# Optimization experiments

Hardware: AMD Instinct MI355X
Metric: run time of the kernel (lower is better)

## Reference

```python
import jax, jax.numpy as jnp
import numpy as np

B, C, N, M, H, L = 2, 128, 6000, 1500, 4, 3
DH = C // H


def conv1(x, W, b):
    # 1x1 Conv1d == per-position matmul: x [B,Cin,N], W [Cout,Cin], b [Cout]
    return jnp.einsum('oc,bcn->bon', W, x) + b[None, :, None]


def setup_inputs():
    key = jax.random.key(0)
    ks = jax.random.split(key, 16)
    w = lambda k, shape, fan: (jax.random.normal(k, shape, jnp.float32) / np.sqrt(fan)).astype(jnp.float32)
    inp = {
        'xs': jax.random.normal(ks[0], (B, 1, N, 4), jnp.float32),
        'd': jax.random.normal(ks[1], (B, C, N), jnp.float32),
        'feat_piece': jax.random.normal(ks[2], (B, C, M), jnp.float32),
        'logits_in': jax.random.normal(ks[3], (B, N), jnp.float32),
        'Wq': w(ks[4], (L, C, C), C), 'bq': jnp.zeros((L, C), jnp.float32),
        'Wk': w(ks[5], (L, C, C), C), 'bk': jnp.zeros((L, C), jnp.float32),
        'Wv': w(ks[6], (L, C, C), C), 'bv': jnp.zeros((L, C), jnp.float32),
        'Wm': w(ks[7], (L, C, C), C), 'bm': jnp.zeros((L, C), jnp.float32),
        'Wc1': w(ks[8], (L, 2 * C, 2 * C), 2 * C), 'bc1': jnp.zeros((L, 2 * C), jnp.float32),
        'bns': jnp.ones((L, 2 * C), jnp.float32), 'bnsh': jnp.zeros((L, 2 * C), jnp.float32),
        'Wc2': w(ks[9], (L, C, 2 * C), 2 * C), 'bc2': jnp.zeros((L, C), jnp.float32),
        'iW1': w(ks[10], (64, C), C), 'ib1': jnp.zeros((64,), jnp.float32),
        'ibn1s': jnp.ones((64,), jnp.float32), 'ibn1sh': jnp.zeros((64,), jnp.float32),
        'iW2': w(ks[11], (16, 64), 64), 'ib2': jnp.zeros((16,), jnp.float32),
        'ibn2s': jnp.ones((16,), jnp.float32), 'ibn2sh': jnp.zeros((16,), jnp.float32),
        'iW3': w(ks[12], (4, 16), 16), 'ib3': jnp.zeros((4,), jnp.float32),
        'ibn3s': jnp.ones((4,), jnp.float32), 'ibn3sh': jnp.zeros((4,), jnp.float32),
        'iW4': w(ks[13], (1, 4), 4), 'ib4': jnp.zeros((1,), jnp.float32),
    }
    return inp


def _forward(xs, d, feat_piece, logits_in, Wq, bq, Wk, bk, Wv, bv, Wm, bm, Wc1, bc1, bns, bnsh, Wc2, bc2,
             iW1, ib1, ibn1s, ibn1sh, iW2, ib2, ibn2s, ibn2sh, iW3, ib3, ibn3s, ibn3sh, iW4, ib4):
    d_old = d
    # kv_mask = (relu(tanh(logits)) > 0) == (logits > 0)
    mask = logits_in > 0.0

    def attention(x1, x2, kv_mask, i):
        bsz = x1.shape[0]
        q = conv1(x1, Wq[i], bq[i]).reshape(bsz, H, DH, -1)  # [B,H,Dh,Nq]
        k = conv1(x2, Wk[i], bk[i]).reshape(bsz, H, DH, -1)  # [B,H,Dh,Nk]
        v = conv1(x2, Wv[i], bv[i]).reshape(bsz, H, DH, -1)
        QK = jnp.einsum('bhdn,bhdm->bhnm', q, k)
        if kv_mask is not None:
            # masked_fill BEFORE the sqrt(head_dim) scaling, as in the original
            QK = jnp.where(kv_mask[:, None, None, :], QK, jnp.float32(-1e6))
        score = jax.nn.softmax(QK / jnp.float32(np.sqrt(DH)), axis=-1)
        add = jnp.einsum('bhnm,bhdm->bhdn', score, v).reshape(bsz, C, -1)
        add = conv1(add, Wm[i], bm[i])
        h = conv1(jnp.concatenate([x1, add], axis=1), Wc1[i], bc1[i])
        # BatchNorm1d (eval) folded into per-channel scale/shift, then ReLU
        h = jax.nn.relu(h * bns[i][None, :, None] + bnsh[i][None, :, None])
        return x1 + conv1(h, Wc2[i], bc2[i])

    feat = attention(feat_piece, d, mask, 0)   # 'cluster':   feat_piece <- d (masked kv)
    feat = attention(feat, feat, None, 1)      # 'context':   self-attention
    d = attention(d, feat, None, 2)            # 'decluster': d <- feat_piece

    def inst_norm(x, eps=1e-3):
        mu = jnp.mean(x, axis=-1, keepdims=True)
        var = jnp.var(x, axis=-1, keepdims=True)  # biased, matches InstanceNorm1d
        return (x - mu) / jnp.sqrt(var + eps)

    def block(x, W, b, s, sh):
        x = inst_norm(conv1(x, W, b))
        return jax.nn.relu(x * s[None, :, None] + sh[None, :, None])

    x = d - d_old
    x = block(x, iW1, ib1, ibn1s, ibn1sh)
    x = block(x, iW2, ib2, ibn2s, ibn2sh)
    x = block(x, iW3, ib3, ibn3s, ibn3sh)
    logits = conv1(x, iW4, ib4)[:, 0, :]  # squeeze channel dim -> [B,N]
    return d, logits  # e_hat is None (loss=False path)


def reference(xs, d, feat_piece, logits_in, Wq, bq, Wk, bk, Wv, bv, Wm, bm, Wc1, bc1, bns, bnsh, Wc2, bc2,
              iW1, ib1, ibn1s, ibn1sh, iW2, ib2, ibn2s, ibn2sh, iW3, ib3, ibn3s, ibn3sh, iW4, ib4):
    return _forward(xs, d, feat_piece, logits_in, Wq, bq, Wk, bk, Wv, bv, Wm, bm, Wc1, bc1, bns, bnsh, Wc2, bc2,
                    iW1, ib1, ibn1s, ibn1sh, iW2, ib2, ibn2s, ibn2sh, iW3, ib3, ibn3s, ibn3sh, iW4, ib4)
```

## Files before the change

kernel.cpp:

```cpp
#include <hip/hip_runtime.h>
#include <math.h>

#define B_  2
#define C_  128
#define N_  6000
#define M_  1500
#define H_  4
#define DH_ 32

typedef __attribute__((ext_vector_type(8))) short bf16x8;
typedef __attribute__((ext_vector_type(4))) float f32x4;
typedef unsigned short u16;

static __device__ __forceinline__ u16 f2bf(float x) {
    unsigned u = __float_as_uint(x);
    return (u16)((u + 0x7fffu + ((u >> 16) & 1u)) >> 16);
}
#define MFMA(a,b,c) __builtin_amdgcn_mfma_f32_16x16x32_bf16((a),(b),(c),0,0,0)
#define INVS2 (0.17677669529663687f * 1.4426950408889634f)

__global__ __launch_bounds__(256) void prep_kernel(
    const float* __restrict__ Wq, const float* __restrict__ Wk, const float* __restrict__ Wv,
    const float* __restrict__ Wm, const float* __restrict__ Wc1, const float* __restrict__ Wc2,
    const float* __restrict__ iW1,
    u16* __restrict__ wq, u16* __restrict__ wk, u16* __restrict__ wv, u16* __restrict__ wm,
    u16* __restrict__ wc1, u16* __restrict__ wc2, u16* __restrict__ w1,
    float* __restrict__ zstats)
{
    long i = (long)blockIdx.x * 256 + threadIdx.x;
    if (i < 512)    zstats[i] = 0.f;
    if (i < 49152)  { wq[i] = f2bf(Wq[i]); wk[i] = f2bf(Wk[i]);
                      wv[i] = f2bf(Wv[i]); wm[i] = f2bf(Wm[i]); }
    if (i < 196608) wc1[i] = f2bf(Wc1[i]);
    if (i < 98304)  wc2[i] = f2bf(Wc2[i]);
    if (i < 8192)   w1[i]  = f2bf(iW1[i]);
}

__global__ __launch_bounds__(256) void qkv_kernel(
    const float* __restrict__ x1, const float* __restrict__ x2, int Pq, int Pk, int Pkpad,
    const u16* __restrict__ wq, const u16* __restrict__ wk, const u16* __restrict__ wv,
    const float* __restrict__ bq, const float* __restrict__ bk, const float* __restrict__ bv,
    u16* __restrict__ Q16, u16* __restrict__ K16, u16* __restrict__ V16)
{
    __shared__ u16 Xt[64][40];
    const int tid = threadIdx.x;
    const int wid = tid >> 6, lane = tid & 63;
    const int l15 = lane & 15, quad = lane >> 4;
    const int job = blockIdx.y >> 1, ot = blockIdx.y & 1;
    const int b = blockIdx.z;
    const int p0 = blockIdx.x * 64;
    const float* X; const u16* W; const float* bias; u16* Y; int P;
    if (job == 0)      { X = x1; W = wq; bias = bq; Y = Q16; P = Pq; }
    else if (job == 1) { X = x2; W = wk; bias = bk; Y = K16; P = Pk; }
    else               { X = x2; W = wv; bias = bv; Y = V16; P = Pk; }
    if (p0 >= P) return;
    const long xoff = (long)b * C_ * P;
    const int sp = tid & 63, cg = tid >> 6;
    f32x4 acc[4] = {};

    for (int k0 = 0; k0 < 128; k0 += 32) {
        bf16x8 st;
        {
            const int pp = (p0 + sp < P) ? p0 + sp : P - 1;
            #pragma unroll
            for (int j = 0; j < 8; ++j)
                st[j] = (short)f2bf(X[xoff + (long)(k0 + cg * 8 + j) * P + pp]);
        }
        __syncthreads();
        *(bf16x8*)&Xt[sp][cg * 8] = st;
        __syncthreads();
        const bf16x8 af = *(const bf16x8*)(W + (long)(ot * 64 + wid * 16 + l15) * 128 + k0 + quad * 8);
        #pragma unroll
        for (int pg = 0; pg < 4; ++pg) {
            const bf16x8 bfr = *(const bf16x8*)&Xt[pg * 16 + l15][quad * 8];
            acc[pg] = MFMA(af, bfr, acc[pg]);
        }
    }
    #pragma unroll
    for (int pg = 0; pg < 4; ++pg)
        #pragma unroll
        for (int r = 0; r < 4; ++r) {
            const int o = ot * 64 + wid * 16 + quad * 4 + r;
            const int p = p0 + pg * 16 + l15;
            if (p < P) {
                const u16 v = f2bf(acc[pg][r] + bias[o]);
                if (job <= 1)
                    Y[((long)(b * 4 + (o >> 5)) * P + p) * 32 + (o & 31)] = v;
                else
                    Y[(long)(b * 128 + o) * Pkpad + p] = v;
            }
        }
}

__global__ __launch_bounds__(256) void attn_partial(
    const u16* __restrict__ Q16, const u16* __restrict__ K16, const u16* __restrict__ V16,
    const float* __restrict__ lgin,
    float* __restrict__ pl, float* __restrict__ pacc,
    int Nq, int Nk, int Nkpad, int KS, int chunkLen)
{
    __shared__ u16 Ps[4][32][72];
    const int tid  = threadIdx.x;
    const int wave = tid >> 6, lane = tid & 63;
    const int l15  = lane & 15, quad = lane >> 4;
    const int bid  = blockIdx.x;
    const int bh   = bid & 7, rest = bid >> 3;
    const int split = rest % KS, qblk = rest / KS;
    const int b = bh >> 2;
    const int q0w = qblk * 128 + wave * 32;

    const u16* Qb = Q16 + (long)bh * Nq * 32;
    const u16* Kb = K16 + (long)bh * Nk * 32;
    const u16* Vb = V16 + (long)(bh * 32) * Nkpad;

    const int qq0 = min(q0w + l15, Nq - 1);
    const int qq1 = min(q0w + 16 + l15, Nq - 1);
    const bf16x8 qa0 = *(const bf16x8*)(Qb + (long)qq0 * 32 + quad * 8);
    const bf16x8 qa1 = *(const bf16x8*)(Qb + (long)qq1 * 32 + quad * 8);

    float lp0 = 0.f, lp1 = 0.f;
    f32x4 o00 = {0.f,0.f,0.f,0.f}, o01 = {0.f,0.f,0.f,0.f};
    f32x4 o10 = {0.f,0.f,0.f,0.f}, o11 = {0.f,0.f,0.f,0.f};

    const int kbeg = split * chunkLen;
    const int kend = min(Nk, kbeg + chunkLen);
    const f32x4 z4 = {0.f,0.f,0.f,0.f};

    for (int m0 = kbeg; m0 < kend; m0 += 64) {
        f32x4 sa0[4], sa1[4];
        #pragma unroll
        for (int kg = 0; kg < 4; ++kg) {
            const int krow = min(m0 + kg * 16 + l15, Nk - 1);
            const bf16x8 ka = *(const bf16x8*)(Kb + (long)krow * 32 + quad * 8);
            sa0[kg] = MFMA(ka, qa0, z4);
            sa1[kg] = MFMA(ka, qa1, z4);
        }

        const int kedge = kend - m0;
        #pragma unroll
        for (int kg = 0; kg < 4; ++kg) {
            float4 mv = {1.f, 1.f, 1.f, 1.f};
            if (lgin)
                mv = *(const float4*)&lgin[(long)b * Nk + min(m0 + kg * 16 + quad * 4, Nk - 4)];
            const float* mr = (const float*)&mv;
            unsigned lo0, hi0, lo1, hi1;
            float p0[4], p1[4];
            #pragma unroll
            for (int r = 0; r < 4; ++r) {
                const bool good = (kg * 16 + quad * 4 + r < kedge) && (mr[r] > 0.f);
                p0[r] = good ? exp2f(sa0[kg][r] * INVS2) : 0.f;
                p1[r] = good ? exp2f(sa1[kg][r] * INVS2) : 0.f;
            }
            lp0 += (p0[0] + p0[1]) + (p0[2] + p0[3]);
            lp1 += (p1[0] + p1[1]) + (p1[2] + p1[3]);
            lo0 = (unsigned)f2bf(p0[0]) | ((unsigned)f2bf(p0[1]) << 16);
            hi0 = (unsigned)f2bf(p0[2]) | ((unsigned)f2bf(p0[3]) << 16);
            lo1 = (unsigned)f2bf(p1[0]) | ((unsigned)f2bf(p1[1]) << 16);
            hi1 = (unsigned)f2bf(p1[2]) | ((unsigned)f2bf(p1[3]) << 16);
            *(uint2*)&Ps[wave][l15][kg * 16 + quad * 4]      = make_uint2(lo0, hi0);
            *(uint2*)&Ps[wave][16 + l15][kg * 16 + quad * 4] = make_uint2(lo1, hi1);
        }

        const bf16x8 pa0lo = *(const bf16x8*)&Ps[wave][l15][quad * 8];
        const bf16x8 pa0hi = *(const bf16x8*)&Ps[wave][l15][32 + quad * 8];
        const bf16x8 pa1lo = *(const bf16x8*)&Ps[wave][16 + l15][quad * 8];
        const bf16x8 pa1hi = *(const bf16x8*)&Ps[wave][16 + l15][32 + quad * 8];
        #pragma unroll
        for (int dg = 0; dg < 2; ++dg) {
            const u16* vrow = Vb + (long)(dg * 16 + l15) * Nkpad + m0;
            const bf16x8 vblo = *(const bf16x8*)(vrow + quad * 8);
            const bf16x8 vbhi = *(const bf16x8*)(vrow + 32 + quad * 8);
            if (dg == 0) {
                o00 = MFMA(pa0lo, vblo, o00); o00 = MFMA(pa0hi, vbhi, o00);
                o10 = MFMA(pa1lo, vblo, o10); o10 = MFMA(pa1hi, vbhi, o10);
            } else {
                o01 = MFMA(pa0lo, vblo, o01); o01 = MFMA(pa0hi, vbhi, o01);
                o11 = MFMA(pa1lo, vblo, o11); o11 = MFMA(pa1hi, vbhi, o11);
            }
        }
    }

    lp0 += __shfl_xor(lp0, 16); lp0 += __shfl_xor(lp0, 32);
    lp1 += __shfl_xor(lp1, 16); lp1 += __shfl_xor(lp1, 32);

    const long base = (long)bh * KS + split;
    if (quad == 0) {
        const int qa = q0w + l15, qbq = q0w + 16 + l15;
        if (qa  < Nq) pl[base * Nq + qa]  = lp0;
        if (qbq < Nq) pl[base * Nq + qbq] = lp1;
    }
    #pragma unroll
    for (int r = 0; r < 4; ++r) {
        const int qa = q0w + quad * 4 + r;
        const int qbq = q0w + 16 + quad * 4 + r;
        if (qa < Nq) {
            float* dst = &pacc[((long)base * Nq + qa) * 32];
            dst[l15] = o00[r]; dst[16 + l15] = o01[r];
        }
        if (qbq < Nq) {
            float* dst = &pacc[((long)base * Nq + qbq) * 32];
            dst[l15] = o10[r]; dst[16 + l15] = o11[r];
        }
    }
}

__global__ __launch_bounds__(256) void epi_kernel(
    const float* __restrict__ pl, const float* __restrict__ pacc, int KS,
    const float* __restrict__ x1,
    const u16* __restrict__ Wm, const float* __restrict__ bm,
    const u16* __restrict__ Wc1, const float* __restrict__ bc1,
    const float* __restrict__ bns, const float* __restrict__ bnsh,
    const u16* __restrict__ Wc2, const float* __restrict__ bc2,
    float* __restrict__ outF, float* __restrict__ outR, int Nq)
{
    __shared__ u16 Xa[32][136];
    __shared__ u16 Xc[32][264];
    __shared__ u16 Xh[32][264];
    const int tid = threadIdx.x;
    const int wid = tid >> 6, lane = tid & 63;
    const int l15 = lane & 15, quad = lane >> 4;
    const int b = blockIdx.y;
    const int p0 = blockIdx.x * 32;

    {
        const int pos = tid & 31, sub = tid >> 5;
        const int pp = (p0 + pos < Nq) ? p0 + pos : Nq - 1;
        const int h = sub >> 1, d0 = (sub & 1) * 16;
        const int bh = b * 4 + h;
        float lg = 0.f, acc[16];
        #pragma unroll
        for (int i = 0; i < 16; ++i) acc[i] = 0.f;
        for (int s = 0; s < KS; ++s) {
            const long base = (long)bh * KS + s;
            lg += pl[base * Nq + pp];
            const float* src = &pacc[(base * Nq + pp) * 32 + d0];
            #pragma unroll
            for (int i = 0; i < 4; ++i) {
                const float4 v = *(const float4*)&src[i * 4];
                acc[i*4+0] += v.x; acc[i*4+1] += v.y; acc[i*4+2] += v.z; acc[i*4+3] += v.w;
            }
        }
        const float inv = 1.f / lg;
        bf16x8 v0, v1;
        #pragma unroll
        for (int i = 0; i < 8; ++i) { v0[i] = (short)f2bf(acc[i] * inv); v1[i] = (short)f2bf(acc[8 + i] * inv); }
        const int c0 = h * 32 + (sub & 1) * 16;
        *(bf16x8*)&Xa[pos][c0] = v0;
        *(bf16x8*)&Xa[pos][c0 + 8] = v1;
        bf16x8 y0, y1;
        #pragma unroll
        for (int j = 0; j < 8; ++j) {
            y0[j] = (short)f2bf(x1[((long)b * 128 + sub * 16 + j) * Nq + pp]);
            y1[j] = (short)f2bf(x1[((long)b * 128 + sub * 16 + 8 + j) * Nq + pp]);
        }
        *(bf16x8*)&Xc[pos][sub * 16] = y0;
        *(bf16x8*)&Xc[pos][sub * 16 + 8] = y1;
    }
    __syncthreads();

    {
        f32x4 am[2][2] = {};
        for (int k0 = 0; k0 < 128; k0 += 32) {
            #pragma unroll
            for (int og = 0; og < 2; ++og) {
                const bf16x8 af = *(const bf16x8*)(Wm + (long)(wid * 32 + og * 16 + l15) * 128 + k0 + quad * 8);
                #pragma unroll
                for (int pg = 0; pg < 2; ++pg) {
                    const bf16x8 bfr = *(const bf16x8*)&Xa[pg * 16 + l15][k0 + quad * 8];
                    am[og][pg] = MFMA(af, bfr, am[og][pg]);
                }
            }
        }
        #pragma unroll
        for (int og = 0; og < 2; ++og)
            #pragma unroll
            for (int pg = 0; pg < 2; ++pg)
                #pragma unroll
                for (int r = 0; r < 4; ++r) {
                    const int o = wid * 32 + og * 16 + quad * 4 + r;
                    Xc[pg * 16 + l15][128 + o] = f2bf(am[og][pg][r] + bm[o]);
                }
    }
    __syncthreads();

    {
        f32x4 a1[4][2] = {};
        for (int k0 = 0; k0 < 256; k0 += 32) {
            #pragma unroll
            for (int og = 0; og < 4; ++og) {
                const bf16x8 af = *(const bf16x8*)(Wc1 + (long)(wid * 64 + og * 16 + l15) * 256 + k0 + quad * 8);
                #pragma unroll
                for (int pg = 0; pg < 2; ++pg) {
                    const bf16x8 bfr = *(const bf16x8*)&Xc[pg * 16 + l15][k0 + quad * 8];
                    a1[og][pg] = MFMA(af, bfr, a1[og][pg]);
                }
            }
        }
        #pragma unroll
        for (int og = 0; og < 4; ++og)
            #pragma unroll
            for (int pg = 0; pg < 2; ++pg)
                #pragma unroll
                for (int r = 0; r < 4; ++r) {
                    const int o = wid * 64 + og * 16 + quad * 4 + r;
                    const float hv = fmaxf((a1[og][pg][r] + bc1[o]) * bns[o] + bnsh[o], 0.f);
                    Xh[pg * 16 + l15][o] = f2bf(hv);
                }
    }
    __syncthreads();

    {
        f32x4 a2[2][2] = {};
        for (int k0 = 0; k0 < 256; k0 += 32) {
            #pragma unroll
            for (int og = 0; og < 2; ++og) {
                const bf16x8 af = *(const bf16x8*)(Wc2 + (long)(wid * 32 + og * 16 + l15) * 256 + k0 + quad * 8);
                #pragma unroll
                for (int pg = 0; pg < 2; ++pg) {
                    const bf16x8 bfr = *(const bf16x8*)&Xh[pg * 16 + l15][k0 + quad * 8];
                    a2[og][pg] = MFMA(af, bfr, a2[og][pg]);
                }
            }
        }
        #pragma unroll
        for (int og = 0; og < 2; ++og)
            #pragma unroll
            for (int pg = 0; pg < 2; ++pg)
                #pragma unroll
                for (int r = 0; r < 4; ++r) {
                    const int o = wid * 32 + og * 16 + quad * 4 + r;
                    const int p = p0 + pg * 16 + l15;
                    if (p < Nq) {
                        const long idx = ((long)b * 128 + o) * Nq + p;
                        const float v = a2[og][pg][r] + bc2[o];
                        outF[idx] = v + x1[idx];
                        if (outR) outR[idx] = v;
                    }
                }
    }
}

__global__ __launch_bounds__(256) void tail1_kernel(
    const float* __restrict__ X, const u16* __restrict__ W, const float* __restrict__ bias,
    float* __restrict__ Y, float* __restrict__ ps, float* __restrict__ pq, int P)
{
    __shared__ u16 Xt[64][40];
    const int tid = threadIdx.x;
    const int wid = tid >> 6, lane = tid & 63;
    const int l15 = lane & 15, quad = lane >> 4;
    const int b = blockIdx.y;
    const int p0 = blockIdx.x * 64;
    const int sp = tid & 63, cg = tid >> 6;
    f32x4 acc[4] = {};
    for (int k0 = 0; k0 < 128; k0 += 32) {
        bf16x8 st;
        {
            const int pp = (p0 + sp < P) ? p0 + sp : P - 1;
            #pragma unroll
            for (int j = 0; j < 8; ++j)
                st[j] = (short)f2bf(X[((long)b * 128 + k0 + cg * 8 + j) * P + pp]);
        }
        __syncthreads();
        *(bf16x8*)&Xt[sp][cg * 8] = st;
        __syncthreads();
        const bf16x8 af = *(const bf16x8*)(W + (long)(wid * 16 + l15) * 128 + k0 + quad * 8);
        #pragma unroll
        for (int pg = 0; pg < 4; ++pg) {
            const bf16x8 bfr = *(const bf16x8*)&Xt[pg * 16 + l15][quad * 8];
            acc[pg] = MFMA(af, bfr, acc[pg]);
        }
    }
    float sums[4] = {}, sq[4] = {};
    #pragma unroll
    for (int pg = 0; pg < 4; ++pg)
        #pragma unroll
        for (int r = 0; r < 4; ++r) {
            const int o = wid * 16 + quad * 4 + r;
            const int p = p0 + pg * 16 + l15;
            if (p < P) {
                const float v = acc[pg][r] + bias[o];
                Y[((long)b * 64 + o) * P + p] = v;
                sums[r] += v; sq[r] += v * v;
            }
        }
    #pragma unroll
    for (int mk = 1; mk < 16; mk <<= 1)
        #pragma unroll
        for (int r = 0; r < 4; ++r) { sums[r] += __shfl_xor(sums[r], mk); sq[r] += __shfl_xor(sq[r], mk); }
    if (l15 == 0)
        #pragma unroll
        for (int r = 0; r < 4; ++r) {
            const int o = wid * 16 + quad * 4 + r;
            atomicAdd(&ps[b * 64 + o], sums[r]);
            atomicAdd(&pq[b * 64 + o], sq[r]);
        }
}

template<int CI, int CO>
__global__ __launch_bounds__(256) void tail_mid(
    const float* __restrict__ xraw, const float* __restrict__ ps, const float* __restrict__ pq,
    const float* __restrict__ sc, const float* __restrict__ sh,
    const float* __restrict__ W, const float* __restrict__ bias,
    float* __restrict__ ps2, float* __restrict__ pq2, float* __restrict__ yraw, int P)
{
    __shared__ float k1s[CI], k2s[CI], Wl[CO * CI];
    const int tid = threadIdx.x;
    const int b = blockIdx.y;
    for (int i = tid; i < CO * CI; i += 256) Wl[i] = W[i];
    if (tid < CI) {
        const float S = ps[b * CI + tid], Q2 = pq[b * CI + tid];
        const float mu = S / P;
        const float var = Q2 / P - mu * mu;
        const float rs = rsqrtf(var + 1e-3f);
        k1s[tid] = rs * sc[tid];
        k2s[tid] = sh[tid] - mu * rs * sc[tid];
    }
    __syncthreads();
    const int p = blockIdx.x * 256 + tid;
    const bool valid = p < P;
    const int pp = valid ? p : P - 1;
    float acc[CO];
    #pragma unroll
    for (int o = 0; o < CO; ++o) acc[o] = bias[o];
    for (int c = 0; c < CI; ++c) {
        const float xn = fmaxf(xraw[((long)b * CI + c) * P + pp] * k1s[c] + k2s[c], 0.f);
        #pragma unroll
        for (int o = 0; o < CO; ++o) acc[o] += Wl[o * CI + c] * xn;
    }
    float sums[CO], sq[CO];
    #pragma unroll
    for (int o = 0; o < CO; ++o) {
        const float v = acc[o];
        if (valid) yraw[((long)b * CO + o) * P + p] = v;
        sums[o] = valid ? v : 0.f;
        sq[o] = valid ? v * v : 0.f;
    }
    #pragma unroll
    for (int mk = 1; mk < 64; mk <<= 1)
        #pragma unroll
        for (int o = 0; o < CO; ++o) { sums[o] += __shfl_xor(sums[o], mk); sq[o] += __shfl_xor(sq[o], mk); }
    if ((tid & 63) == 0)
        #pragma unroll
        for (int o = 0; o < CO; ++o) {
            atomicAdd(&ps2[b * CO + o], sums[o]);
            atomicAdd(&pq2[b * CO + o], sq[o]);
        }
}

__global__ __launch_bounds__(256) void tail4_kernel(
    const float* __restrict__ xraw, const float* __restrict__ ps, const float* __restrict__ pq,
    const float* __restrict__ sc, const float* __restrict__ sh,
    const float* __restrict__ W4, const float* __restrict__ b4,
    float* __restrict__ out, int P)
{
    const int tid = threadIdx.x;
    const int b = blockIdx.y;
    const int p = blockIdx.x * 256 + tid;
    if (p >= P) return;
    float acc = b4[0];
    #pragma unroll
    for (int c = 0; c < 4; ++c) {
        const float S = ps[b * 4 + c], Q2 = pq[b * 4 + c];
        const float mu = S / P;
        const float var = Q2 / P - mu * mu;
        const float rs = rsqrtf(var + 1e-3f);
        const float k1 = rs * sc[c], k2 = sh[c] - mu * rs * sc[c];
        const float xn = fmaxf(xraw[((long)b * 4 + c) * P + p] * k1 + k2, 0.f);
        acc += W4[c] * xn;
    }
    out[(long)b * P + p] = acc;
}

extern "C" void kernel_launch(void* const* d_in, const int* in_sizes, int n_in,
                              void* d_out, int out_size, void* d_ws, size_t ws_size,
                              hipStream_t stream)
{
    const float* dX   = (const float*)d_in[1];
    const float* fpX  = (const float*)d_in[2];
    const float* lgin = (const float*)d_in[3];
    const float* Wq = (const float*)d_in[4];  const float* bq = (const float*)d_in[5];
    const float* Wk = (const float*)d_in[6];  const float* bk = (const float*)d_in[7];
    const float* Wv = (const float*)d_in[8];  const float* bv = (const float*)d_in[9];
    const float* Wm = (const float*)d_in[10]; const float* bm = (const float*)d_in[11];
    const float* Wc1= (const float*)d_in[12]; const float* bc1= (const float*)d_in[13];
    const float* bns= (const float*)d_in[14]; const float* bnsh=(const float*)d_in[15];
    const float* Wc2= (const float*)d_in[16]; const float* bc2= (const float*)d_in[17];
    const float* iW1= (const float*)d_in[18]; const float* ib1= (const float*)d_in[19];
    const float* s1 = (const float*)d_in[20]; const float* h1 = (const float*)d_in[21];
    const float* iW2= (const float*)d_in[22]; const float* ib2= (const float*)d_in[23];
    const float* s2 = (const float*)d_in[24]; const float* h2 = (const float*)d_in[25];
    const float* iW3= (const float*)d_in[26]; const float* ib3= (const float*)d_in[27];
    const float* s3 = (const float*)d_in[28]; const float* h3 = (const float*)d_in[29];
    const float* iW4= (const float*)d_in[30]; const float* ib4= (const float*)d_in[31];

    float* out_d      = (float*)d_out;
    float* out_logits = out_d + (long)B_ * C_ * N_;

    float* f = (float*)d_ws;
    long off = 0;
    auto alloc = [&](long n) { float* p = f + off; off += n; return p; };
    float* featA = alloc(384000);
    float* featB = alloc(384000);
    float* q16f  = alloc(800000);
    float* k16f  = alloc(800000);
    float* v16f  = alloc(800000);
    float* xb    = alloc(1536000);
    float* x1raw = alloc(768000);
    float* x2raw = alloc(192000);
    float* x3raw = alloc(48000);
    float* plb   = alloc(100000);
    float* pacc  = alloc(3200000);
    float* zst   = alloc(512);
    float* wreg  = alloc(250000);
    (void)ws_size; (void)in_sizes; (void)n_in; (void)out_size;

    float* ps1 = zst;        float* pq1 = zst + 128;
    float* ps2 = zst + 256;  float* pq2 = zst + 288;
    float* ps3 = zst + 320;  float* pq3 = zst + 328;

    u16* wq_h  = (u16*)wreg;
    u16* wk_h  = wq_h + 49152;
    u16* wv_h  = wk_h + 49152;
    u16* wm_h  = wv_h + 49152;
    u16* wc1_h = wm_h + 49152;
    u16* wc2_h = wc1_h + 196608;
    u16* w1_h  = wc2_h + 98304;

    u16* Q16 = (u16*)q16f;
    u16* K16 = (u16*)k16f;
    u16* V16 = (u16*)v16f;

    prep_kernel<<<dim3(768), 256, 0, stream>>>(Wq, Wk, Wv, Wm, Wc1, Wc2, iW1,
                                               wq_h, wk_h, wv_h, wm_h, wc1_h, wc2_h, w1_h, zst);

    auto layer = [&](const float* x1, const float* x2, int Nq, int Nk,
                     const float* maskl, int li, int KS, int chunkLen,
                     float* outF, float* outR) {
        const int Nkpad = ((Nk + 63) & ~63) + 64;
        qkv_kernel<<<dim3((max(Nq, Nk) + 63) / 64, 6, B_), 256, 0, stream>>>(
            x1, x2, Nq, Nk, Nkpad,
            wq_h + (long)li * 16384, wk_h + (long)li * 16384, wv_h + (long)li * 16384,
            bq + li * 128, bk + li * 128, bv + li * 128, Q16, K16, V16);
        const int qblocks = (Nq + 127) / 128;
        attn_partial<<<dim3(qblocks * KS * 8), 256, 0, stream>>>(
            Q16, K16, V16, maskl, plb, pacc, Nq, Nk, Nkpad, KS, chunkLen);
        epi_kernel<<<dim3((Nq + 31) / 32, B_), 256, 0, stream>>>(
            plb, pacc, KS, x1,
            wm_h + (long)li * 16384, bm + li * 128,
            wc1_h + (long)li * 65536, bc1 + li * 256, bns + li * 256, bnsh + li * 256,
            wc2_h + (long)li * 32768, bc2 + li * 128,
            outF, outR, Nq);
    };

    layer(fpX,   dX,    M_, N_, lgin,    0, 8, 768, featA, nullptr);
    layer(featA, featA, M_, M_, nullptr, 1, 8, 192, featB, nullptr);
    layer(dX,    featB, N_, M_, nullptr, 2, 2, 768, out_d, xb);

    tail1_kernel<<<dim3((N_ + 63) / 64, B_), 256, 0, stream>>>(xb, w1_h, ib1, x1raw, ps1, pq1, N_);
    tail_mid<64, 16><<<dim3((N_ + 255) / 256, B_), 256, 0, stream>>>(
        x1raw, ps1, pq1, s1, h1, iW2, ib2, ps2, pq2, x2raw, N_);
    tail_mid<16, 4><<<dim3((N_ + 255) / 256, B_), 256, 0, stream>>>(
        x2raw, ps2, pq2, s2, h2, iW3, ib3, ps3, pq3, x3raw, N_);
    tail4_kernel<<<dim3((N_ + 255) / 256, B_), 256, 0, stream>>>(
        x3raw, ps3, pq3, s3, h3, iW4, ib4, out_logits, N_);
}
```

Baseline: 397.8 us.

## Pad K/V to chunk multiple, fold softmax scale into Q, row sums via MFMA

The QKV projection now pre-scales Q by the softmax/log2 factor and writes K and V zero-padded to KS*chunkLen. V gets an extra block of rows with a ones row appended. The attention kernel drops the per-element bounds clamps and scale multiply, uses a template to skip the mask path when unmasked, and truncates P to bf16 instead of rounding it. Row sums are computed with extra MFMAs against a ones fragment instead of VALU adds and shuffles, with padded keys subtracted as npad (exp(0)=1). This trades more memory traffic, extra MFMAs and a slight precision change for less VALU work in the inner loop.

```diff
diff --git a/kernel.cpp b/kernel.cpp
--- a/kernel.cpp
+++ b/kernel.cpp
@@ -49,54 +49,71 @@
     const int job = blockIdx.y >> 1, ot = blockIdx.y & 1;
     const int b = blockIdx.z;
     const int p0 = blockIdx.x * 64;
-    const float* X; const u16* W; const float* bias; u16* Y; int P;
-    if (job == 0)      { X = x1; W = wq; bias = bq; Y = Q16; P = Pq; }
-    else if (job == 1) { X = x2; W = wk; bias = bk; Y = K16; P = Pk; }
-    else               { X = x2; W = wv; bias = bv; Y = V16; P = Pk; }
-    if (p0 >= P) return;
-    const long xoff = (long)b * C_ * P;
-    const int sp = tid & 63, cg = tid >> 6;
-    f32x4 acc[4] = {};
-
-    for (int k0 = 0; k0 < 128; k0 += 32) {
-        bf16x8 st;
-        {
-            const int pp = (p0 + sp < P) ? p0 + sp : P - 1;
-            #pragma unroll
-            for (int j = 0; j < 8; ++j)
-                st[j] = (short)f2bf(X[xoff + (long)(k0 + cg * 8 + j) * P + pp]);
-        }
-        __syncthreads();
-        *(bf16x8*)&Xt[sp][cg * 8] = st;
-        __syncthreads();
-        const bf16x8 af = *(const bf16x8*)(W + (long)(ot * 64 + wid * 16 + l15) * 128 + k0 + quad * 8);
-        #pragma unroll
-        for (int pg = 0; pg < 4; ++pg) {
-            const bf16x8 bfr = *(const bf16x8*)&Xt[pg * 16 + l15][quad * 8];
-            acc[pg] = MFMA(af, bfr, acc[pg]);
-        }
-    }
-    #pragma unroll
-    for (int pg = 0; pg < 4; ++pg)
-        #pragma unroll
-        for (int r = 0; r < 4; ++r) {
-            const int o = ot * 64 + wid * 16 + quad * 4 + r;
-            const int p = p0 + pg * 16 + l15;
-            if (p < P) {
-                const u16 v = f2bf(acc[pg][r] + bias[o]);
-                if (job <= 1)
-                    Y[((long)(b * 4 + (o >> 5)) * P + p) * 32 + (o & 31)] = v;
-                else
-                    Y[(long)(b * 128 + o) * Pkpad + p] = v;
-            }
-        }
-}
-
+    const float* X; const u16* W; const float* bias; int P;
+    if (job == 0)      { X = x1; W = wq; bias = bq; P = Pq; }
+    else if (job == 1) { X = x2; W = wk; bias = bk; P = Pk; }
+    else               { X = x2; W = wv; bias = bv; P = Pk; }
+    const int Plim = (job == 0) ? Pq : Pkpad;
+    if (p0 < Plim) {
+        const long xoff = (long)b * C_ * P;
+        const int sp = tid & 63, cg = tid >> 6;
+        f32x4 acc[4] = {};
+        if (p0 < P) {
+            for (int k0 = 0; k0 < 128; k0 += 32) {
+                bf16x8 st;
+                const int pp = (p0 + sp < P) ? p0 + sp : P - 1;
+                #pragma unroll
+                for (int j = 0; j < 8; ++j)
+                    st[j] = (short)f2bf(X[xoff + (long)(k0 + cg * 8 + j) * P + pp]);
+                __syncthreads();
+                *(bf16x8*)&Xt[sp][cg * 8] = st;
+                __syncthreads();
+                const bf16x8 af = *(const bf16x8*)(W + (long)(ot * 64 + wid * 16 + l15) * 128 + k0 + quad * 8);
+                #pragma unroll
+                for (int pg = 0; pg < 4; ++pg) {
+                    const bf16x8 bfr = *(const bf16x8*)&Xt[pg * 16 + l15][quad * 8];
+                    acc[pg] = MFMA(af, bfr, acc[pg]);
+                }
+            }
+        }
+        #pragma unroll
+        for (int pg = 0; pg < 4; ++pg)
+            #pragma unroll
+            for (int r = 0; r < 4; ++r) {
+                const int o = ot * 64 + wid * 16 + quad * 4 + r;
+                const int p = p0 + pg * 16 + l15;
+                if (p >= Plim) continue;
+                if (job == 0) {
+                    if (p < Pq)
+                        Q16[((long)(b * 4 + (o >> 5)) * Pq + p) * 32 + (o & 31)] =
+                            f2bf((acc[pg][r] + bias[o]) * INVS2);
+                } else {
+                    const u16 v = (p < P) ? f2bf(acc[pg][r] + bias[o]) : (u16)0;
+                    if (job == 1)
+                        K16[((long)(b * 4 + (o >> 5)) * Pkpad + p) * 32 + (o & 31)] = v;
+                    else
+                        V16[((long)(b * 4 + (o >> 5)) * 48 + (o & 31)) * Pkpad + p] = v;
+                }
+            }
+        if (job == 2) {
+            for (int e = tid; e < 2048; e += 256) {
+                const int which = e >> 10;
+                const int row = 32 + ((e >> 6) & 15);
+                const int col = p0 + (e & 63);
+                if (col < Pkpad)
+                    V16[((long)(b * 4 + ot * 2 + which) * 48 + row) * Pkpad + col] =
+                        (row == 32) ? (u16)0x3F80 : (u16)0;
+            }
+        }
+    }
+}
+
+template<bool MASKED>
 __global__ __launch_bounds__(256) void attn_partial(
     const u16* __restrict__ Q16, const u16* __restrict__ K16, const u16* __restrict__ V16,
     const float* __restrict__ lgin,
     float* __restrict__ pl, float* __restrict__ pacc,
-    int Nq, int Nk, int Nkpad, int KS, int chunkLen)
+    int Nq, int Nk, int Nkpad, int KS, int chunkLen, int npad)
 {
     __shared__ u16 Ps[4][32][72];
     const int tid  = threadIdx.x;
@@ -109,97 +126,90 @@
     const int q0w = qblk * 128 + wave * 32;
 
     const u16* Qb = Q16 + (long)bh * Nq * 32;
-    const u16* Kb = K16 + (long)bh * Nk * 32;
-    const u16* Vb = V16 + (long)(bh * 32) * Nkpad;
+    const u16* Kb = K16 + (long)bh * Nkpad * 32;
+    const u16* Vb = V16 + (long)(bh * 48) * Nkpad;
 
     const int qq0 = min(q0w + l15, Nq - 1);
     const int qq1 = min(q0w + 16 + l15, Nq - 1);
     const bf16x8 qa0 = *(const bf16x8*)(Qb + (long)qq0 * 32 + quad * 8);
     const bf16x8 qa1 = *(const bf16x8*)(Qb + (long)qq1 * 32 + quad * 8);
 
-    float lp0 = 0.f, lp1 = 0.f;
-    f32x4 o00 = {0.f,0.f,0.f,0.f}, o01 = {0.f,0.f,0.f,0.f};
-    f32x4 o10 = {0.f,0.f,0.f,0.f}, o11 = {0.f,0.f,0.f,0.f};
+    bf16x8 onesf;
+    #pragma unroll
+    for (int j = 0; j < 8; ++j) onesf[j] = (short)(l15 == 0 ? 0x3F80 : 0);
+
+    f32x4 o00={0,0,0,0}, o01={0,0,0,0}, o10={0,0,0,0}, o11={0,0,0,0};
+    f32x4 ol0={0,0,0,0}, ol1={0,0,0,0};
+    const f32x4 z4 = {0,0,0,0};
 
     const int kbeg = split * chunkLen;
-    const int kend = min(Nk, kbeg + chunkLen);
-    const f32x4 z4 = {0.f,0.f,0.f,0.f};
+    const int kend = kbeg + chunkLen;
 
     for (int m0 = kbeg; m0 < kend; m0 += 64) {
         f32x4 sa0[4], sa1[4];
         #pragma unroll
         for (int kg = 0; kg < 4; ++kg) {
-            const int krow = min(m0 + kg * 16 + l15, Nk - 1);
-            const bf16x8 ka = *(const bf16x8*)(Kb + (long)krow * 32 + quad * 8);
+            const bf16x8 ka = *(const bf16x8*)(Kb + (long)(m0 + kg * 16 + l15) * 32 + quad * 8);
             sa0[kg] = MFMA(ka, qa0, z4);
             sa1[kg] = MFMA(ka, qa1, z4);
         }
-
-        const int kedge = kend - m0;
         #pragma unroll
         for (int kg = 0; kg < 4; ++kg) {
-            float4 mv = {1.f, 1.f, 1.f, 1.f};
-            if (lgin)
-                mv = *(const float4*)&lgin[(long)b * Nk + min(m0 + kg * 16 + quad * 4, Nk - 4)];
-            const float* mr = (const float*)&mv;
-            unsigned lo0, hi0, lo1, hi1;
             float p0[4], p1[4];
-            #pragma unroll
-            for (int r = 0; r < 4; ++r) {
-                const bool good = (kg * 16 + quad * 4 + r < kedge) && (mr[r] > 0.f);
-                p0[r] = good ? exp2f(sa0[kg][r] * INVS2) : 0.f;
-                p1[r] = good ? exp2f(sa1[kg][r] * INVS2) : 0.f;
-            }
-            lp0 += (p0[0] + p0[1]) + (p0[2] + p0[3]);
-            lp1 += (p1[0] + p1[1]) + (p1[2] + p1[3]);
-            lo0 = (unsigned)f2bf(p0[0]) | ((unsigned)f2bf(p0[1]) << 16);
-            hi0 = (unsigned)f2bf(p0[2]) | ((unsigned)f2bf(p0[3]) << 16);
-            lo1 = (unsigned)f2bf(p1[0]) | ((unsigned)f2bf(p1[1]) << 16);
-            hi1 = (unsigned)f2bf(p1[2]) | ((unsigned)f2bf(p1[3]) << 16);
-            *(uint2*)&Ps[wave][l15][kg * 16 + quad * 4]      = make_uint2(lo0, hi0);
-            *(uint2*)&Ps[wave][16 + l15][kg * 16 + quad * 4] = make_uint2(lo1, hi1);
-        }
-
+            if (MASKED) {
+                const int kbase = m0 + kg * 16 + quad * 4;
+                const float4 mv = *(const float4*)&lgin[(long)b * Nk + min(kbase, Nk - 4)];
+                const float* mr = (const float*)&mv;
+                #pragma unroll
+                for (int r = 0; r < 4; ++r) {
+                    const bool good = (kbase + r < Nk) && (mr[r] > 0.f);
+                    p0[r] = good ? exp2f(sa0[kg][r]) : 0.f;
+                    p1[r] = good ? exp2f(sa1[kg][r]) : 0.f;
+                }
+            } else {
+                #pragma unroll
+                for (int r = 0; r < 4; ++r) { p0[r] = exp2f(sa0[kg][r]); p1[r] = exp2f(sa1[kg][r]); }
+            }
+            const unsigned a0 = (__float_as_uint(p0[0]) >> 16) | (__float_as_uint(p0[1]) & 0xffff0000u);
+            const unsigned a1 = (__float_as_uint(p0[2]) >> 16) | (__float_as_uint(p0[3]) & 0xffff0000u);
+            const unsigned b0 = (__float_as_uint(p1[0]) >> 16) | (__float_as_uint(p1[1]) & 0xffff0000u);
+            const unsigned b1 = (__float_as_uint(p1[2]) >> 16) | (__float_as_uint(p1[3]) & 0xffff0000u);
+            *(uint2*)&Ps[wave][l15][kg * 16 + quad * 4]      = make_uint2(a0, a1);
+            *(uint2*)&Ps[wave][16 + l15][kg * 16 + quad * 4] = make_uint2(b0, b1);
+        }
         const bf16x8 pa0lo = *(const bf16x8*)&Ps[wave][l15][quad * 8];
         const bf16x8 pa0hi = *(const bf16x8*)&Ps[wave][l15][32 + quad * 8];
         const bf16x8 pa1lo = *(const bf16x8*)&Ps[wave][16 + l15][quad * 8];
         const bf16x8 pa1hi = *(const bf16x8*)&Ps[wave][16 + l15][32 + quad * 8];
-        #pragma unroll
-        for (int dg = 0; dg < 2; ++dg) {
-            const u16* vrow = Vb + (long)(dg * 16 + l15) * Nkpad + m0;
-            const bf16x8 vblo = *(const bf16x8*)(vrow + quad * 8);
-            const bf16x8 vbhi = *(const bf16x8*)(vrow + 32 + quad * 8);
-            if (dg == 0) {
-                o00 = MFMA(pa0lo, vblo, o00); o00 = MFMA(pa0hi, vbhi, o00);
-                o10 = MFMA(pa1lo, vblo, o10); o10 = MFMA(pa1hi, vbhi, o10);
-            } else {
-                o01 = MFMA(pa0lo, vblo, o01); o01 = MFMA(pa0hi, vbhi, o01);
-                o11 = MFMA(pa1lo, vblo, o11); o11 = MFMA(pa1hi, vbhi, o11);
-            }
-        }
-    }
-
-    lp0 += __shfl_xor(lp0, 16); lp0 += __shfl_xor(lp0, 32);
-    lp1 += __shfl_xor(lp1, 16); lp1 += __shfl_xor(lp1, 32);
+        const u16* vr0 = Vb + (long)l15 * Nkpad + m0;
+        const u16* vr1 = Vb + (long)(16 + l15) * Nkpad + m0;
+        const bf16x8 v0lo = *(const bf16x8*)(vr0 + quad * 8);
+        const bf16x8 v0hi = *(const bf16x8*)(vr0 + 32 + quad * 8);
+        const bf16x8 v1lo = *(const bf16x8*)(vr1 + quad * 8);
+        const bf16x8 v1hi = *(const bf16x8*)(vr1 + 32 + quad * 8);
+        o00 = MFMA(pa0lo, v0lo, o00); o00 = MFMA(pa0hi, v0hi, o00);
+        o01 = MFMA(pa0lo, v1lo, o01); o01 = MFMA(pa0hi, v1hi, o01);
+        o10 = MFMA(pa1lo, v0lo, o10); o10 = MFMA(pa1hi, v0hi, o10);
+        o11 = MFMA(pa1lo, v1lo, o11); o11 = MFMA(pa1hi, v1hi, o11);
+        ol0 = MFMA(pa0lo, onesf, ol0); ol0 = MFMA(pa0hi, onesf, ol0);
+        ol1 = MFMA(pa1lo, onesf, ol1); ol1 = MFMA(pa1hi, onesf, ol1);
+    }
 
     const long base = (long)bh * KS + split;
-    if (quad == 0) {
-        const int qa = q0w + l15, qbq = q0w + 16 + l15;
-        if (qa  < Nq) pl[base * Nq + qa]  = lp0;
-        if (qbq < Nq) pl[base * Nq + qbq] = lp1;
+    const float fn = (split == KS - 1) ? (float)npad : 0.f;
+    if (l15 == 0) {
+        #pragma unroll
+        for (int r = 0; r < 4; ++r) {
+            const int qA = q0w + quad * 4 + r, qB = qA + 16;
+            if (qA < Nq) pl[base * Nq + qA] = ol0[r] - fn;
+            if (qB < Nq) pl[base * Nq + qB] = ol1[r] - fn;
+        }
     }
     #pragma unroll
     for (int r = 0; r < 4; ++r) {
-        const int qa = q0w + quad * 4 + r;
-        const int qbq = q0w + 16 + quad * 4 + r;
-        if (qa < Nq) {
-            float* dst = &pacc[((long)base * Nq + qa) * 32];
-            dst[l15] = o00[r]; dst[16 + l15] = o01[r];
-        }
-        if (qbq < Nq) {
-            float* dst = &pacc[((long)base * Nq + qbq) * 32];
-            dst[l15] = o10[r]; dst[16 + l15] = o11[r];
-        }
+        const int qA = q0w + quad * 4 + r, qB = qA + 16;
+        if (qA < Nq) { float* d = &pacc[((long)base * Nq + qA) * 32]; d[l15] = o00[r]; d[16 + l15] = o01[r]; }
+        if (qB < Nq) { float* d = &pacc[((long)base * Nq + qB) * 32]; d[l15] = o10[r]; d[16 + l15] = o11[r]; }
     }
 }
 
@@ -502,7 +512,7 @@
     float* featB = alloc(384000);
     float* q16f  = alloc(800000);
     float* k16f  = alloc(800000);
-    float* v16f  = alloc(800000);
+    float* v16f  = alloc(1200000);
     float* xb    = alloc(1536000);
     float* x1raw = alloc(768000);
     float* x2raw = alloc(192000);
@@ -535,14 +545,19 @@
     auto layer = [&](const float* x1, const float* x2, int Nq, int Nk,
                      const float* maskl, int li, int KS, int chunkLen,
                      float* outF, float* outR) {
-        const int Nkpad = ((Nk + 63) & ~63) + 64;
-        qkv_kernel<<<dim3((max(Nq, Nk) + 63) / 64, 6, B_), 256, 0, stream>>>(
+        const int Nkpad = KS * chunkLen;
+        const int npad  = maskl ? 0 : (Nkpad - Nk);
+        qkv_kernel<<<dim3((max(Nq, Nkpad) + 63) / 64, 6, B_), 256, 0, stream>>>(
             x1, x2, Nq, Nk, Nkpad,
             wq_h + (long)li * 16384, wk_h + (long)li * 16384, wv_h + (long)li * 16384,
             bq + li * 128, bk + li * 128, bv + li * 128, Q16, K16, V16);
         const int qblocks = (Nq + 127) / 128;
-        attn_partial<<<dim3(qblocks * KS * 8), 256, 0, stream>>>(
-            Q16, K16, V16, maskl, plb, pacc, Nq, Nk, Nkpad, KS, chunkLen);
+        if (maskl)
+            attn_partial<true><<<dim3(qblocks * KS * 8), 256, 0, stream>>>(
+                Q16, K16, V16, maskl, plb, pacc, Nq, Nk, Nkpad, KS, chunkLen, npad);
+        else
+            attn_partial<false><<<dim3(qblocks * KS * 8), 256, 0, stream>>>(
+                Q16, K16, V16, nullptr, plb, pacc, Nq, Nk, Nkpad, KS, chunkLen, npad);
         epi_kernel<<<dim3((Nq + 31) / 32, B_), 256, 0, stream>>>(
             plb, pacc, KS, x1,
             wm_h + (long)li * 16384, bm + li * 128,
```

New measurement: 395.6 us. About the same (-0.6%).
